# Performance work log

Hardware: AMD Instinct MI355X
Metric: run time of the kernel (lower is better)

The kernel has to match this reference:

```python
import jax, jax.numpy as jnp
import numpy as np


def setup_inputs() -> dict:
    key = jax.random.key(0)
    H, W, C, N = 200, 200, 256, 2000
    img = jax.random.normal(key, (1, H, W, C), dtype=jnp.float32)
    rng = np.random.RandomState(0)
    x = rng.randint(0, W - 50, size=N)
    y = rng.randint(0, H - 50, size=N)
    w = rng.randint(8, 50, size=N)
    h = rng.randint(8, 50, size=N)
    rois = jnp.asarray(np.stack([x, y, w, h], axis=-1)[None].astype(np.float32))
    return {"img": img, "rois": rois, "pool_size": 7}


def _roi_bilinear(feat, roi, ps):
    # feat: (H, W, C); roi: int32 (x, y, w, h) -> (ps, ps, C)
    # Mirrors TF1 tf.image.resize_images bilinear, align_corners=False:
    # src coordinate inside the crop = out_idx * (crop_size / ps).
    H, W = feat.shape[0], feat.shape[1]
    x, y, w, h = roi[0], roi[1], roi[2], roi[3]
    sy = h.astype(jnp.float32) / ps
    sx = w.astype(jnp.float32) / ps
    src_y = jnp.arange(ps, dtype=jnp.float32) * sy
    src_x = jnp.arange(ps, dtype=jnp.float32) * sx
    y0 = jnp.floor(src_y).astype(jnp.int32)
    x0 = jnp.floor(src_x).astype(jnp.int32)
    wy = src_y - y0.astype(jnp.float32)
    wx = src_x - x0.astype(jnp.float32)
    # clamp inside the crop, then translate to global image coords (and clamp for safety)
    gy0 = jnp.clip(y + jnp.clip(y0, 0, h - 1), 0, H - 1)
    gy1 = jnp.clip(y + jnp.clip(y0 + 1, 0, h - 1), 0, H - 1)
    gx0 = jnp.clip(x + jnp.clip(x0, 0, w - 1), 0, W - 1)
    gx1 = jnp.clip(x + jnp.clip(x0 + 1, 0, w - 1), 0, W - 1)
    v00 = feat[gy0[:, None], gx0[None, :]]  # (ps, ps, C)
    v01 = feat[gy0[:, None], gx1[None, :]]
    v10 = feat[gy1[:, None], gx0[None, :]]
    v11 = feat[gy1[:, None], gx1[None, :]]
    wy = wy[:, None, None]
    wx = wx[None, :, None]
    top = v00 * (1.0 - wx) + v01 * wx
    bot = v10 * (1.0 - wx) + v11 * wx
    return top * (1.0 - wy) + bot * wy


def reference(img, rois, pool_size):
    feat = img[0]                          # (H, W, C)
    roi_int = rois[0].astype(jnp.int32)    # (N, 4) -- cast as in the 'tf' branch
    pooled = jax.vmap(lambda r: _roi_bilinear(feat, r, pool_size))(roi_int)
    return pooled[None]                    # (1, N, ps, ps, C)
```

## Files before the change

### kernel.cpp

```cpp
#include <hip/hip_runtime.h>
#include <hip/hip_bf16.h>


__global__ __launch_bounds__(256) void RoIPool_53575422050620_kernel(
    const float* __restrict__ feat,
    const float* __restrict__ rois,
    const int*   __restrict__ psp,
    float*       __restrict__ out,
    int n_cells, int H, int W, int C)
{
    const int ps   = psp[0];
    const int cell = blockIdx.x * 4 + (threadIdx.x >> 6);
    if (cell >= n_cells) return;
    const int lane = threadIdx.x & 63;

    const int pp  = ps * ps;
    const int roi = cell / pp;
    const int rem = cell - roi * pp;
    const int py  = rem / ps;
    const int px  = rem - py * ps;

    const float4 r = reinterpret_cast<const float4*>(rois)[roi];
    const int x = (int)r.x;
    const int y = (int)r.y;
    const int w = (int)r.z;
    const int h = (int)r.w;

    const float sy    = (float)h / (float)ps;
    const float sx    = (float)w / (float)ps;
    const float src_y = (float)py * sy;
    const float src_x = (float)px * sx;
    const int y0 = (int)floorf(src_y);
    const int x0 = (int)floorf(src_x);
    const float wy = src_y - (float)y0;
    const float wx = src_x - (float)x0;

    const int gy0 = min(max(y + min(max(y0,     0), h - 1), 0), H - 1);
    const int gy1 = min(max(y + min(max(y0 + 1, 0), h - 1), 0), H - 1);
    const int gx0 = min(max(x + min(max(x0,     0), w - 1), 0), W - 1);
    const int gx1 = min(max(x + min(max(x0 + 1, 0), w - 1), 0), W - 1);

    const int C4 = C >> 2;
    const float4* __restrict__ f4 = reinterpret_cast<const float4*>(feat);
    float4* __restrict__ o4 = reinterpret_cast<float4*>(out);

    const size_t b00 = (size_t)(gy0 * W + gx0) * C4;
    const size_t b01 = (size_t)(gy0 * W + gx1) * C4;
    const size_t b10 = (size_t)(gy1 * W + gx0) * C4;
    const size_t b11 = (size_t)(gy1 * W + gx1) * C4;
    const size_t ob  = (size_t)cell * C4;

    const float omwx = 1.0f - wx;
    const float omwy = 1.0f - wy;

    for (int cv = lane; cv < C4; cv += 64) {
        const float4 v00 = f4[b00 + cv];
        const float4 v01 = f4[b01 + cv];
        const float4 v10 = f4[b10 + cv];
        const float4 v11 = f4[b11 + cv];
        float4 o;
        o.x = (v00.x * omwx + v01.x * wx) * omwy + (v10.x * omwx + v11.x * wx) * wy;
        o.y = (v00.y * omwx + v01.y * wx) * omwy + (v10.y * omwx + v11.y * wx) * wy;
        o.z = (v00.z * omwx + v01.z * wx) * omwy + (v10.z * omwx + v11.z * wx) * wy;
        o.w = (v00.w * omwx + v01.w * wx) * omwy + (v10.w * omwx + v11.w * wx) * wy;
        o4[ob + cv] = o;
    }
}

extern "C" void kernel_launch(void* const* d_in, const int* in_sizes, int n_in,
                              void* d_out, int out_size, void* d_ws, size_t ws_size,
                              hipStream_t stream) {
    const float* img  = (const float*)d_in[0];
    const float* rois = (const float*)d_in[1];
    const int*   psp  = (const int*)d_in[2];
    float*       out  = (float*)d_out;

    const int H = 200, W = 200, C = 256;
    const int n_cells = out_size / C;
    const int blocks  = (n_cells + 3) / 4;

    RoIPool_53575422050620_kernel<<<blocks, 256, 0, stream>>>(
        img, rois, psp, out, n_cells, H, W, C);
}
```

Baseline: 166.7 us.

## Add per-RoI row kernel specialized for pool size 7 with batched loads

Adds a templated kernel that assigns one block per RoI and one wavefront per output row. Each lane issues all 28 gathers for its row up front, which raises memory-level parallelism and drops the per-cell division and psp reads. Stores are nontemporal to avoid polluting cache with output. Pool size is inferred from the buffer sizes on the host, with a fallback to the old kernel; it holds many float4 registers per thread and launches only 2000 blocks.

```diff
diff --git a/kernel.cpp b/kernel.cpp
--- a/kernel.cpp
+++ b/kernel.cpp
@@ -1,5 +1,72 @@
 #include <hip/hip_runtime.h>
-#include <hip/hip_bf16.h>
+
+
+typedef float vfloat4 __attribute__((ext_vector_type(4)));
+
+template <int PS>
+__global__ __launch_bounds__(PS * 64) void RoIPool_rows_kernel(
+    const float* __restrict__ feat,
+    const float* __restrict__ rois,
+    float*       __restrict__ out,
+    int H, int W)
+{
+    constexpr int C4 = 64;
+    const int roi  = blockIdx.x;
+    const int py   = threadIdx.x >> 6;
+    const int lane = threadIdx.x & 63;
+
+    const float4 r = reinterpret_cast<const float4*>(rois)[roi];
+    const int x = (int)r.x;
+    const int y = (int)r.y;
+    const int w = (int)r.z;
+    const int h = (int)r.w;
+
+    const float sy = (float)h / (float)PS;
+    const float sx = (float)w / (float)PS;
+
+    const float src_y = (float)py * sy;
+    const int   y0    = (int)floorf(src_y);
+    const float wy    = src_y - (float)y0;
+    const float omwy  = 1.0f - wy;
+    const int gy0 = min(max(y + min(max(y0,     0), h - 1), 0), H - 1);
+    const int gy1 = min(max(y + min(max(y0 + 1, 0), h - 1), 0), H - 1);
+
+    const float4* __restrict__ f4 = reinterpret_cast<const float4*>(feat);
+
+    const int rb0 = gy0 * W * C4 + lane;
+    const int rb1 = gy1 * W * C4 + lane;
+
+    float4 v00[PS], v01[PS], v10[PS], v11[PS];
+    float  wxa[PS];
+
+#pragma unroll
+    for (int px = 0; px < PS; ++px) {
+        const float src_x = (float)px * sx;
+        const int   x0    = (int)floorf(src_x);
+        wxa[px] = src_x - (float)x0;
+        const int gx0 = min(max(x + min(max(x0,     0), w - 1), 0), W - 1);
+        const int gx1 = min(max(x + min(max(x0 + 1, 0), w - 1), 0), W - 1);
+        v00[px] = f4[rb0 + gx0 * C4];
+        v01[px] = f4[rb0 + gx1 * C4];
+        v10[px] = f4[rb1 + gx0 * C4];
+        v11[px] = f4[rb1 + gx1 * C4];
+    }
+
+    vfloat4* __restrict__ o4 = reinterpret_cast<vfloat4*>(out);
+    const int ob = (roi * (PS * PS) + py * PS) * C4 + lane;
+
+#pragma unroll
+    for (int px = 0; px < PS; ++px) {
+        const float wx   = wxa[px];
+        const float omwx = 1.0f - wx;
+        vfloat4 o;
+        o.x = (v00[px].x * omwx + v01[px].x * wx) * omwy + (v10[px].x * omwx + v11[px].x * wx) * wy;
+        o.y = (v00[px].y * omwx + v01[px].y * wx) * omwy + (v10[px].y * omwx + v11[px].y * wx) * wy;
+        o.z = (v00[px].z * omwx + v01[px].z * wx) * omwy + (v10[px].z * omwx + v11[px].z * wx) * wy;
+        o.w = (v00[px].w * omwx + v01[px].w * wx) * omwy + (v10[px].w * omwx + v11[px].w * wx) * wy;
+        __builtin_nontemporal_store(o, o4 + ob + px * C4);
+    }
+}
 
 
 __global__ __launch_bounds__(256) void RoIPool_53575422050620_kernel(
@@ -77,8 +144,16 @@
 
     const int H = 200, W = 200, C = 256;
     const int n_cells = out_size / C;
-    const int blocks  = (n_cells + 3) / 4;
+    const int N  = in_sizes[1] / 4;
+    const int pp = (N > 0) ? (n_cells / N) : 0;
+    int ps = 1;
+    while (ps * ps < pp) ++ps;
 
-    RoIPool_53575422050620_kernel<<<blocks, 256, 0, stream>>>(
-        img, rois, psp, out, n_cells, H, W, C);
+    if (N > 0 && pp == 49 && ps * ps == pp && ps * ps * N == n_cells && C == 256) {
+        RoIPool_rows_kernel<7><<<N, 7 * 64, 0, stream>>>(img, rois, out, H, W);
+    } else {
+        const int blocks = (n_cells + 3) / 4;
+        RoIPool_53575422050620_kernel<<<blocks, 256, 0, stream>>>(
+            img, rois, psp, out, n_cells, H, W, C);
+    }
 }
```

New measurement: 169.1 us. No clear change (+1.4%).
